# Optimization experiments

Hardware: AMD Instinct MI355X
Metric: run time of the kernel (lower is better)

The kernel has to match this reference:

```python
import jax, jax.numpy as jnp
import numpy as np

D_MODEL = 1024
D_FF = 4096
LN_EPS = 1e-5


def _layer_norm(x, gamma, beta):
    mu = jnp.mean(x, axis=-1, keepdims=True)
    var = jnp.mean(jnp.square(x - mu), axis=-1, keepdims=True)
    return (x - mu) * jax.lax.rsqrt(var + LN_EPS) * gamma + beta


def setup_inputs() -> dict:
    key = jax.random.key(0)
    ks = jax.random.split(key, 16)
    B, S, D, F = 2, 2048, D_MODEL, D_FF
    s_d = 1.0 / np.sqrt(D)
    s_f = 1.0 / np.sqrt(F)
    u = lambda k, shape, s: jax.random.uniform(k, shape, jnp.float32, -s, s)
    return {
        "x": jax.random.normal(ks[0], (B, S, D), jnp.float32),
        "wq": u(ks[1], (D, D), s_d), "bq": u(ks[2], (D,), s_d),
        "wk": u(ks[3], (D, D), s_d), "bk": u(ks[4], (D,), s_d),
        "wv": u(ks[5], (D, D), s_d), "bv": u(ks[6], (D,), s_d),
        "wo": u(ks[7], (D, D), s_d), "bo": u(ks[8], (D,), s_d),
        "w1": u(ks[9], (F, D), s_d), "b1": u(ks[10], (F,), s_d),
        "w2": u(ks[11], (D, F), s_f), "b2": u(ks[12], (D,), s_f),
        "g1": jnp.ones((D,), jnp.float32), "be1": jnp.zeros((D,), jnp.float32),
        "g2": jnp.ones((D,), jnp.float32), "be2": jnp.zeros((D,), jnp.float32),
        "num_heads": 16,
    }


def reference(x, wq, bq, wk, bk, wv, bv, wo, bo, w1, b1, w2, b2, g1, be1, g2, be2, num_heads):
    B, S, D = x.shape
    H = num_heads
    dk = D // H
    scale = 1.0 / np.sqrt(dk)

    # --- self-attention (pre-norm) ---
    h = _layer_norm(x, g1, be1)
    q = (h @ wq.T + bq).reshape(B, S, H, dk)
    k = (h @ wk.T + bk).reshape(B, S, H, dk)
    v = (h @ wv.T + bv).reshape(B, S, H, dk)
    scores = jnp.einsum("bqhd,bkhd->bhqk", q, k) * scale  # [B,H,S,S]
    attn = jax.nn.softmax(scores, axis=-1)
    ctx = jnp.einsum("bhqk,bkhd->bqhd", attn, v).reshape(B, S, D)
    x = x + ctx @ wo.T + bo

    # --- feed-forward (pre-norm, exact GELU as in torch default) ---
    h = _layer_norm(x, g2, be2)
    h = jax.nn.gelu(h @ w1.T + b1, approximate=False)
    x = x + h @ w2.T + b2
    return x
```

## Files before the change

### kernel.cpp

```cpp
#include <hip/hip_runtime.h>

typedef __attribute__((ext_vector_type(8))) __bf16 bf16x8;
typedef __attribute__((ext_vector_type(4))) __bf16 bf16x4;
typedef __attribute__((ext_vector_type(4))) float floatx4;
typedef void __attribute__((address_space(3))) lds_void_t;
typedef const void __attribute__((address_space(1))) gbl_void_t;

#define D_MODEL 1024
#define SEQ     2048
#define BATCH   2
#define NH      16
#define DK      64
#define DFF     4096
#define NTOK    (BATCH * SEQ)
#define QKVS    3072

#if __has_builtin(__builtin_amdgcn_exp2f)
#define EXP2(x) __builtin_amdgcn_exp2f(x)
#else
#define EXP2(x) exp2f(x)
#endif

__device__ __forceinline__ float gelu_exact(float x) {
    return 0.5f * x * (1.0f + erff(x * 0.70710678118654752f));
}

__global__ __launch_bounds__(256) void cast_f32_bf16(const float* __restrict__ src,
                                                     __bf16* __restrict__ dst, int n) {
    int i = (blockIdx.x * 256 + threadIdx.x) * 8;
    if (i >= n) return;
    floatx4 a = *(const floatx4*)(src + i);
    floatx4 b = *(const floatx4*)(src + i + 4);
    bf16x8 o;
    for (int j = 0; j < 4; ++j) { o[j] = (__bf16)a[j]; o[4 + j] = (__bf16)b[j]; }
    *(bf16x8*)(dst + i) = o;
}

__global__ __launch_bounds__(64) void ln_kernel(const float* __restrict__ x,
                                                const float* __restrict__ g,
                                                const float* __restrict__ b,
                                                __bf16* __restrict__ out) {
    int row = blockIdx.x, lane = threadIdx.x, base = lane * 16;
    const float* xr = x + (size_t)row * D_MODEL + base;
    float v[16];
    for (int j = 0; j < 4; ++j) {
        floatx4 a = *(const floatx4*)(xr + 4 * j);
        for (int i = 0; i < 4; ++i) v[4 * j + i] = a[i];
    }
    float s = 0.f, sq = 0.f;
    for (int i = 0; i < 16; ++i) { s += v[i]; sq += v[i] * v[i]; }
    for (int o = 1; o < 64; o <<= 1) { s += __shfl_xor(s, o); sq += __shfl_xor(sq, o); }
    float mu = s * (1.0f / D_MODEL);
    float var = sq * (1.0f / D_MODEL) - mu * mu;
    float rstd = rsqrtf(fmaxf(var, 0.f) + 1e-5f);

    const floatx4* gp = (const floatx4*)(g + base);
    const floatx4* bp = (const floatx4*)(b + base);
    bf16x8 o0, o1;
    for (int j = 0; j < 2; ++j) {
        floatx4 gv0 = gp[2 * j], gv1 = gp[2 * j + 1];
        floatx4 bv0 = bp[2 * j], bv1 = bp[2 * j + 1];
        for (int i = 0; i < 4; ++i) {
            float r0 = (v[8 * j + i] - mu) * rstd * gv0[i] + bv0[i];
            float r1 = (v[8 * j + 4 + i] - mu) * rstd * gv1[i] + bv1[i];
            if (j == 0) { o0[i] = (__bf16)r0; o0[4 + i] = (__bf16)r1; }
            else        { o1[i] = (__bf16)r0; o1[4 + i] = (__bf16)r1; }
        }
    }
    bf16x8* op = (bf16x8*)(out + (size_t)row * D_MODEL + base);
    op[0] = o0; op[1] = o1;
}

template <typename OutT, bool GELU, bool TRIBIAS, int KSPLIT>
__global__ __launch_bounds__(256) void gemm_bt(const __bf16* __restrict__ A,
                                               const __bf16* __restrict__ W,
                                               const float* __restrict__ bias0,
                                               const float* __restrict__ bias1,
                                               const float* __restrict__ bias2,
                                               const float* __restrict__ res,
                                               OutT* out, float* part1,
                                               int M, int N, int K) {
    __shared__ __bf16 As[2][128][32];
    __shared__ __bf16 Ws[2][128][32];

    int m0 = blockIdx.y * 128, n0 = blockIdx.x * 128;
    int t = threadIdx.x;
    int lane = t & 63, wave = t >> 6;
    int wm = (wave >> 1) * 64, wn = (wave & 1) * 64;
    int fr = lane & 15, quad = lane >> 4;
    int srow = t >> 2, scol = (t & 3) * 8;

    int Ks = K / KSPLIT;
    int kbeg = (KSPLIT > 1) ? blockIdx.z * Ks : 0;

    floatx4 acc[4][4] = {};

    const __bf16* Ab = A + (size_t)(m0 + srow) * K + kbeg + scol;
    const __bf16* Wb = W + (size_t)(n0 + srow) * K + kbeg + scol;

    auto stage = [&](int buf, int k0) {
        __builtin_amdgcn_global_load_lds((gbl_void_t*)(Ab + k0),
                                         (lds_void_t*)&As[buf][wave * 16][0], 16, 0, 0);
        __builtin_amdgcn_global_load_lds((gbl_void_t*)(Ab + (size_t)64 * K + k0),
                                         (lds_void_t*)&As[buf][64 + wave * 16][0], 16, 0, 0);
        __builtin_amdgcn_global_load_lds((gbl_void_t*)(Wb + k0),
                                         (lds_void_t*)&Ws[buf][wave * 16][0], 16, 0, 0);
        __builtin_amdgcn_global_load_lds((gbl_void_t*)(Wb + (size_t)64 * K + k0),
                                         (lds_void_t*)&Ws[buf][64 + wave * 16][0], 16, 0, 0);
    };

    stage(0, 0);
    int nsteps = Ks / 32;
    for (int s = 0; s < nsteps; ++s) {
        int cur = s & 1;
        __syncthreads();
        if (s + 1 < nsteps) stage(cur ^ 1, (s + 1) * 32);

        bf16x8 af[4], wf[4];
#pragma unroll
        for (int i = 0; i < 4; ++i) af[i] = *(const bf16x8*)&As[cur][wm + i * 16 + fr][quad * 8];
#pragma unroll
        for (int i = 0; i < 4; ++i) wf[i] = *(const bf16x8*)&Ws[cur][wn + i * 16 + fr][quad * 8];
#pragma unroll
        for (int mi = 0; mi < 4; ++mi)
#pragma unroll
            for (int ni = 0; ni < 4; ++ni)
                acc[mi][ni] = __builtin_amdgcn_mfma_f32_16x16x32_bf16(af[mi], wf[ni], acc[mi][ni], 0, 0, 0);
    }

    if (KSPLIT > 1) {
        float* pb = (blockIdx.z == 0) ? (float*)out : part1;
#pragma unroll
        for (int ni = 0; ni < 4; ++ni) {
            int col = n0 + wn + ni * 16 + fr;
#pragma unroll
            for (int mi = 0; mi < 4; ++mi)
#pragma unroll
                for (int r = 0; r < 4; ++r) {
                    int row = m0 + wm + mi * 16 + quad * 4 + r;
                    pb[(size_t)row * N + col] = acc[mi][ni][r];
                }
        }
    } else {
#pragma unroll
        for (int ni = 0; ni < 4; ++ni) {
            int col = n0 + wn + ni * 16 + fr;
            const float* bp = bias0;
            int bcol = col;
            if (TRIBIAS) { bp = col < 1024 ? bias0 : (col < 2048 ? bias1 : bias2); bcol = col & 1023; }
            float bv = bp[bcol];
#pragma unroll
            for (int mi = 0; mi < 4; ++mi) {
#pragma unroll
                for (int r = 0; r < 4; ++r) {
                    int row = m0 + wm + mi * 16 + quad * 4 + r;
                    float v = acc[mi][ni][r] + bv;
                    if (GELU) v = gelu_exact(v);
                    if (res) v += res[(size_t)row * N + col];
                    out[(size_t)row * N + col] = (OutT)v;
                }
            }
        }
    }
}

__global__ __launch_bounds__(256) void reduce_k2(const float* __restrict__ p0,
                                                 const float* p1,
                                                 const float* __restrict__ res,
                                                 const float* __restrict__ bias,
                                                 float* out) {
    int i = (blockIdx.x * 256 + threadIdx.x) * 4;
    floatx4 a = *(const floatx4*)(p0 + i);
    floatx4 b = *(const floatx4*)(p1 + i);
    floatx4 r = *(const floatx4*)(res + i);
    floatx4 bv = *(const floatx4*)(bias + (i & 1023));
    floatx4 o;
#pragma unroll
    for (int j = 0; j < 4; ++j) o[j] = a[j] + b[j] + r[j] + bv[j];
    *(floatx4*)(out + i) = o;
}

__global__ __launch_bounds__(256) void transpose_v(const __bf16* __restrict__ qkv,
                                                   __bf16* __restrict__ vt) {
    __shared__ __bf16 tile[64][72];
    int b = blockIdx.z, h = blockIdx.y, s0 = blockIdx.x * 64;
    int t = threadIdx.x;
    int dl = (t & 7) * 8, sl = t >> 3;
    for (int p = 0; p < 2; ++p) {
        int s = sl + p * 32;
        bf16x8 val = *(const bf16x8*)(qkv + (size_t)(b * SEQ + s0 + s) * QKVS + 2048 + h * DK + dl);
        *(bf16x8*)&tile[s][dl] = val;
    }
    __syncthreads();
    int sl2 = (t & 7) * 8, d = t >> 3;
    for (int p = 0; p < 2; ++p) {
        int dd = d + p * 32;
        bf16x8 val;
        for (int j = 0; j < 8; ++j) val[j] = tile[sl2 + j][dd];
        *(bf16x8*)(vt + ((size_t)(b * NH + h) * DK + dd) * SEQ + s0 + sl2) = val;
    }
}

__global__ __launch_bounds__(256, 2) void attn_kernel(const __bf16* __restrict__ qkv,
                                                      const __bf16* __restrict__ vt,
                                                      __bf16* __restrict__ ctx) {
    __shared__ __bf16 Klds[8192];
    __shared__ __bf16 Vlds[8192];
    __shared__ __bf16 Plds[4][16][136];
    int b = blockIdx.z, h = blockIdx.y;
    int wave = threadIdx.x >> 6, lane = threadIdx.x & 63;
    int q0 = blockIdx.x * 64 + wave * 16;
    int fr = lane & 15, quad = lane >> 4;
    const float sc2 = 0.18033688011112042f;

    const __bf16* qp = qkv + (size_t)(b * SEQ + q0 + fr) * QKVS + h * DK + quad * 8;
    bf16x8 qf0 = *(const bf16x8*)qp;
    bf16x8 qf1 = *(const bf16x8*)(qp + 32);

    const __bf16* kg = qkv + (size_t)b * SEQ * QKVS + 1024 + h * DK;
    const __bf16* vg = vt + (size_t)(b * NH + h) * DK * SEQ;

    floatx4 o[4] = {};
    float m_i = -1e30f, l_i = 0.f;

    auto stage_tile = [&](int k0) {
#pragma unroll
        for (int p = 0; p < 4; ++p) {
            int bid = wave * 4 + p;
            int f = bid >> 1, half = bid & 1;
            __builtin_amdgcn_global_load_lds(
                (gbl_void_t*)(kg + (size_t)(k0 + f * 16 + fr) * QKVS + quad * 8 + half * 32),
                (lds_void_t*)&Klds[bid * 512], 16, 0, 0);
            int c = bid >> 2, ti = bid & 3;
            __builtin_amdgcn_global_load_lds(
                (gbl_void_t*)(vg + (size_t)(ti * 16 + fr) * SEQ + k0 + c * 32 + quad * 8),
                (lds_void_t*)&Vlds[bid * 512], 16, 0, 0);
        }
    };

    stage_tile(0);
    __syncthreads();

    for (int k0 = 0; k0 < SEQ; k0 += 128) {
        const __bf16* Kb = Klds + lane * 8;
        const __bf16* Vb = Vlds + lane * 8;
        bf16x8 kA[8], kB[8];
#pragma unroll
        for (int f = 0; f < 8; ++f) {
            kA[f] = *(const bf16x8*)(Kb + (f * 2 + 0) * 512);
            kB[f] = *(const bf16x8*)(Kb + (f * 2 + 1) * 512);
        }
        bf16x8 vf[4][4];
#pragma unroll
        for (int c = 0; c < 4; ++c)
#pragma unroll
            for (int ti = 0; ti < 4; ++ti)
                vf[c][ti] = *(const bf16x8*)(Vb + (c * 4 + ti) * 512);
        __syncthreads();

        if (k0 + 128 < SEQ) stage_tile(k0 + 128);

        floatx4 s[8];
#pragma unroll
        for (int f = 0; f < 8; ++f) {
            floatx4 z = {0.f, 0.f, 0.f, 0.f};
            z = __builtin_amdgcn_mfma_f32_16x16x32_bf16(kA[f], qf0, z, 0, 0, 0);
            s[f] = __builtin_amdgcn_mfma_f32_16x16x32_bf16(kB[f], qf1, z, 0, 0, 0);
        }

        float fm[8];
#pragma unroll
        for (int f = 0; f < 8; ++f)
            fm[f] = fmaxf(fmaxf(s[f][0], s[f][1]), fmaxf(s[f][2], s[f][3]));
        float mx = fmaxf(fmaxf(fmaxf(fm[0], fm[1]), fmaxf(fm[2], fm[3])),
                         fmaxf(fmaxf(fm[4], fm[5]), fmaxf(fm[6], fm[7])));
        float mx2 = mx * sc2;
        mx2 = fmaxf(mx2, __shfl_xor(mx2, 16));
        mx2 = fmaxf(mx2, __shfl_xor(mx2, 32));
        float mn = fmaxf(m_i, mx2);
        float alpha = EXP2(m_i - mn);
        m_i = mn;
        float r0 = 0.f, r1 = 0.f, r2 = 0.f, r3 = 0.f;
#pragma unroll
        for (int f = 0; f < 8; ++f) {
            bf16x4 pk;
            float p0 = EXP2(fmaf(s[f][0], sc2, -mn));
            float p1 = EXP2(fmaf(s[f][1], sc2, -mn));
            float p2 = EXP2(fmaf(s[f][2], sc2, -mn));
            float p3 = EXP2(fmaf(s[f][3], sc2, -mn));
            r0 += p0; r1 += p1; r2 += p2; r3 += p3;
            pk[0] = (__bf16)p0; pk[1] = (__bf16)p1; pk[2] = (__bf16)p2; pk[3] = (__bf16)p3;
            *(bf16x4*)&Plds[wave][fr][f * 16 + quad * 4] = pk;
        }
        float rs = (r0 + r1) + (r2 + r3);
        rs += __shfl_xor(rs, 16);
        rs += __shfl_xor(rs, 32);
        l_i = l_i * alpha + rs;
        float aB[4];
#pragma unroll
        for (int r = 0; r < 4; ++r) aB[r] = __shfl(alpha, quad * 4 + r);
#pragma unroll
        for (int ti = 0; ti < 4; ++ti)
#pragma unroll
            for (int r = 0; r < 4; ++r) o[ti][r] *= aB[r];
        __threadfence_block();

        bf16x8 pa[4];
#pragma unroll
        for (int c = 0; c < 4; ++c)
            pa[c] = *(const bf16x8*)&Plds[wave][fr][c * 32 + quad * 8];
#pragma unroll
        for (int c = 0; c < 4; ++c)
#pragma unroll
            for (int ti = 0; ti < 4; ++ti)
                o[ti] = __builtin_amdgcn_mfma_f32_16x16x32_bf16(pa[c], vf[c][ti], o[ti], 0, 0, 0);
        __threadfence_block();

        __syncthreads();
    }
    float lB[4];
#pragma unroll
    for (int r = 0; r < 4; ++r) lB[r] = __shfl(l_i, quad * 4 + r);
#pragma unroll
    for (int ti = 0; ti < 4; ++ti)
#pragma unroll
        for (int r = 0; r < 4; ++r)
            ctx[(size_t)(b * SEQ + q0 + quad * 4 + r) * D_MODEL + h * DK + ti * 16 + fr] =
                (__bf16)(o[ti][r] / lB[r]);
}

extern "C" void kernel_launch(void* const* d_in, const int* in_sizes, int n_in,
                              void* d_out, int out_size, void* d_ws, size_t ws_size,
                              hipStream_t stream) {
    const float* x   = (const float*)d_in[0];
    const float* wq  = (const float*)d_in[1];
    const float* bq  = (const float*)d_in[2];
    const float* wk  = (const float*)d_in[3];
    const float* bk  = (const float*)d_in[4];
    const float* wv  = (const float*)d_in[5];
    const float* bv  = (const float*)d_in[6];
    const float* wo  = (const float*)d_in[7];
    const float* bo  = (const float*)d_in[8];
    const float* w1  = (const float*)d_in[9];
    const float* b1  = (const float*)d_in[10];
    const float* w2  = (const float*)d_in[11];
    const float* b2  = (const float*)d_in[12];
    const float* g1  = (const float*)d_in[13];
    const float* be1 = (const float*)d_in[14];
    const float* g2  = (const float*)d_in[15];
    const float* be2 = (const float*)d_in[16];
    float* out = (float*)d_out;

    char* ws = (char*)d_ws;
    const size_t MB = 1024 * 1024;
    __bf16* wqkvB = (__bf16*)(ws);
    __bf16* woB   = (__bf16*)(ws + 6 * MB);
    __bf16* w1B   = (__bf16*)(ws + 8 * MB);
    __bf16* w2B   = (__bf16*)(ws + 16 * MB);
    __bf16* h1    = (__bf16*)(ws + 24 * MB);
    float*  x1    = (float*)(ws + 24 * MB);
    __bf16* qkv   = (__bf16*)(ws + 40 * MB);
    __bf16* vt    = (__bf16*)(ws + 64 * MB);
    __bf16* ffh   = (__bf16*)(ws + 40 * MB);
    float*  pA0   = (float*)(ws + 40 * MB);
    float*  pA1   = (float*)(ws + 56 * MB);
    float*  pF0   = (float*)(ws);
    __bf16* ctx   = (__bf16*)d_out;
    __bf16* h2    = (__bf16*)d_out;

    const int NDD = D_MODEL * D_MODEL;
    const int NDF = D_MODEL * DFF;
    cast_f32_bf16<<<NDD / 2048, 256, 0, stream>>>(wq, wqkvB, NDD);
    cast_f32_bf16<<<NDD / 2048, 256, 0, stream>>>(wk, wqkvB + NDD, NDD);
    cast_f32_bf16<<<NDD / 2048, 256, 0, stream>>>(wv, wqkvB + 2 * NDD, NDD);
    cast_f32_bf16<<<NDD / 2048, 256, 0, stream>>>(wo, woB, NDD);
    cast_f32_bf16<<<NDF / 2048, 256, 0, stream>>>(w1, w1B, NDF);
    cast_f32_bf16<<<NDF / 2048, 256, 0, stream>>>(w2, w2B, NDF);

    dim3 gQKV(QKVS / 128, NTOK / 128);
    dim3 gDz(D_MODEL / 128, NTOK / 128, 2);
    dim3 gF(DFF / 128, NTOK / 128);
    dim3 gAttn(SEQ / 64, NH, BATCH);
    int gRed = NTOK * D_MODEL / (256 * 4);

    ln_kernel<<<NTOK, 64, 0, stream>>>(x, g1, be1, h1);
    gemm_bt<__bf16, false, true, 1><<<gQKV, 256, 0, stream>>>(h1, wqkvB, bq, bk, bv, nullptr, qkv, nullptr, NTOK, QKVS, D_MODEL);
    transpose_v<<<gAttn, 256, 0, stream>>>(qkv, vt);
    attn_kernel<<<gAttn, 256, 0, stream>>>(qkv, vt, ctx);
    gemm_bt<float, false, false, 2><<<gDz, 256, 0, stream>>>(ctx, woB, nullptr, nullptr, nullptr, nullptr, pA0, pA1, NTOK, D_MODEL, D_MODEL);
    reduce_k2<<<gRed, 256, 0, stream>>>(pA0, pA1, x, bo, x1);
    ln_kernel<<<NTOK, 64, 0, stream>>>(x1, g2, be2, h2);
    gemm_bt<__bf16, true, false, 1><<<gF, 256, 0, stream>>>(h2, w1B, b1, b1, b1, nullptr, ffh, nullptr, NTOK, DFF, D_MODEL);
    gemm_bt<float, false, false, 2><<<gDz, 256, 0, stream>>>(ffh, w2B, nullptr, nullptr, nullptr, nullptr, pF0, (float*)d_out, NTOK, D_MODEL, DFF);
    reduce_k2<<<gRed, 256, 0, stream>>>(pF0, (float*)d_out, x1, b2, out);
}
```

Measured before the change: 432.3 us.

## Process two 16-row query tiles per wave in attention to reuse K/V fragments

Each attention wave now handles 32 query rows as two 16-row subtiles instead of 16, so the block covers 128 queries and the grid halves. K and V fragments loaded from LDS per 128-key tile are reused across both subtiles, halving LDS and global K/V traffic per query. Part of the second subtile's QK MFMAs are placed before the barrier to overlap with the softmax. This raises register pressure (more accumulators and score arrays) and leaves fewer blocks (512) to fill the GPU.

```diff
diff --git a/kernel.cpp b/kernel.cpp
--- a/kernel.cpp
+++ b/kernel.cpp
@@ -206,22 +206,23 @@
                                                       __bf16* __restrict__ ctx) {
     __shared__ __bf16 Klds[8192];
     __shared__ __bf16 Vlds[8192];
-    __shared__ __bf16 Plds[4][16][136];
+    __shared__ __bf16 Plds[4][32][136];
     int b = blockIdx.z, h = blockIdx.y;
     int wave = threadIdx.x >> 6, lane = threadIdx.x & 63;
-    int q0 = blockIdx.x * 64 + wave * 16;
+    int q0 = blockIdx.x * 128 + wave * 32;
     int fr = lane & 15, quad = lane >> 4;
     const float sc2 = 0.18033688011112042f;
 
-    const __bf16* qp = qkv + (size_t)(b * SEQ + q0 + fr) * QKVS + h * DK + quad * 8;
-    bf16x8 qf0 = *(const bf16x8*)qp;
-    bf16x8 qf1 = *(const bf16x8*)(qp + 32);
+    const __bf16* qp0 = qkv + (size_t)(b * SEQ + q0 + fr) * QKVS + h * DK + quad * 8;
+    const __bf16* qp1 = qp0 + (size_t)16 * QKVS;
+    bf16x8 qA0 = *(const bf16x8*)qp0, qB0 = *(const bf16x8*)(qp0 + 32);
+    bf16x8 qA1 = *(const bf16x8*)qp1, qB1 = *(const bf16x8*)(qp1 + 32);
 
     const __bf16* kg = qkv + (size_t)b * SEQ * QKVS + 1024 + h * DK;
     const __bf16* vg = vt + (size_t)(b * NH + h) * DK * SEQ;
 
-    floatx4 o[4] = {};
-    float m_i = -1e30f, l_i = 0.f;
+    floatx4 o[8] = {};
+    float m0q = -1e30f, l0q = 0.f, m1q = -1e30f, l1q = 0.f;
 
     auto stage_tile = [&](int k0) {
 #pragma unroll
@@ -250,83 +251,141 @@
             kA[f] = *(const bf16x8*)(Kb + (f * 2 + 0) * 512);
             kB[f] = *(const bf16x8*)(Kb + (f * 2 + 1) * 512);
         }
+
+        floatx4 s[8];
+#pragma unroll
+        for (int f = 0; f < 8; ++f) {
+            floatx4 z = {0.f, 0.f, 0.f, 0.f};
+            z = __builtin_amdgcn_mfma_f32_16x16x32_bf16(kA[f], qA0, z, 0, 0, 0);
+            s[f] = __builtin_amdgcn_mfma_f32_16x16x32_bf16(kB[f], qB0, z, 0, 0, 0);
+        }
+        {
+            float fm[8];
+#pragma unroll
+            for (int f = 0; f < 8; ++f)
+                fm[f] = fmaxf(fmaxf(s[f][0], s[f][1]), fmaxf(s[f][2], s[f][3]));
+            float mx = fmaxf(fmaxf(fmaxf(fm[0], fm[1]), fmaxf(fm[2], fm[3])),
+                             fmaxf(fmaxf(fm[4], fm[5]), fmaxf(fm[6], fm[7])));
+            float mx2 = mx * sc2;
+            mx2 = fmaxf(mx2, __shfl_xor(mx2, 16));
+            mx2 = fmaxf(mx2, __shfl_xor(mx2, 32));
+            float mn = fmaxf(m0q, mx2);
+            float alpha = EXP2(m0q - mn);
+            m0q = mn;
+            float r0 = 0.f, r1 = 0.f, r2 = 0.f, r3 = 0.f;
+#pragma unroll
+            for (int f = 0; f < 8; ++f) {
+                bf16x4 pk;
+                float p0 = EXP2(fmaf(s[f][0], sc2, -mn));
+                float p1 = EXP2(fmaf(s[f][1], sc2, -mn));
+                float p2 = EXP2(fmaf(s[f][2], sc2, -mn));
+                float p3 = EXP2(fmaf(s[f][3], sc2, -mn));
+                r0 += p0; r1 += p1; r2 += p2; r3 += p3;
+                pk[0] = (__bf16)p0; pk[1] = (__bf16)p1; pk[2] = (__bf16)p2; pk[3] = (__bf16)p3;
+                *(bf16x4*)&Plds[wave][fr][f * 16 + quad * 4] = pk;
+            }
+            float rs = (r0 + r1) + (r2 + r3);
+            rs += __shfl_xor(rs, 16);
+            rs += __shfl_xor(rs, 32);
+            l0q = l0q * alpha + rs;
+            float aB[4];
+#pragma unroll
+            for (int r = 0; r < 4; ++r) aB[r] = __shfl(alpha, quad * 4 + r);
+#pragma unroll
+            for (int ti = 0; ti < 4; ++ti)
+#pragma unroll
+                for (int r = 0; r < 4; ++r) o[ti][r] *= aB[r];
+        }
+
+        floatx4 s1[8];
+#pragma unroll
+        for (int f = 0; f < 8; ++f) {
+            floatx4 z = {0.f, 0.f, 0.f, 0.f};
+            z = __builtin_amdgcn_mfma_f32_16x16x32_bf16(kA[f], qA1, z, 0, 0, 0);
+            s1[f] = __builtin_amdgcn_mfma_f32_16x16x32_bf16(kB[f], qB1, z, 0, 0, 0);
+        }
+
         bf16x8 vf[4][4];
 #pragma unroll
         for (int c = 0; c < 4; ++c)
 #pragma unroll
             for (int ti = 0; ti < 4; ++ti)
                 vf[c][ti] = *(const bf16x8*)(Vb + (c * 4 + ti) * 512);
+
         __syncthreads();
-
         if (k0 + 128 < SEQ) stage_tile(k0 + 128);
 
-        floatx4 s[8];
-#pragma unroll
-        for (int f = 0; f < 8; ++f) {
-            floatx4 z = {0.f, 0.f, 0.f, 0.f};
-            z = __builtin_amdgcn_mfma_f32_16x16x32_bf16(kA[f], qf0, z, 0, 0, 0);
-            s[f] = __builtin_amdgcn_mfma_f32_16x16x32_bf16(kB[f], qf1, z, 0, 0, 0);
-        }
-
-        float fm[8];
-#pragma unroll
-        for (int f = 0; f < 8; ++f)
-            fm[f] = fmaxf(fmaxf(s[f][0], s[f][1]), fmaxf(s[f][2], s[f][3]));
-        float mx = fmaxf(fmaxf(fmaxf(fm[0], fm[1]), fmaxf(fm[2], fm[3])),
-                         fmaxf(fmaxf(fm[4], fm[5]), fmaxf(fm[6], fm[7])));
-        float mx2 = mx * sc2;
-        mx2 = fmaxf(mx2, __shfl_xor(mx2, 16));
-        mx2 = fmaxf(mx2, __shfl_xor(mx2, 32));
-        float mn = fmaxf(m_i, mx2);
-        float alpha = EXP2(m_i - mn);
-        m_i = mn;
-        float r0 = 0.f, r1 = 0.f, r2 = 0.f, r3 = 0.f;
-#pragma unroll
-        for (int f = 0; f < 8; ++f) {
-            bf16x4 pk;
-            float p0 = EXP2(fmaf(s[f][0], sc2, -mn));
-            float p1 = EXP2(fmaf(s[f][1], sc2, -mn));
-            float p2 = EXP2(fmaf(s[f][2], sc2, -mn));
-            float p3 = EXP2(fmaf(s[f][3], sc2, -mn));
-            r0 += p0; r1 += p1; r2 += p2; r3 += p3;
-            pk[0] = (__bf16)p0; pk[1] = (__bf16)p1; pk[2] = (__bf16)p2; pk[3] = (__bf16)p3;
-            *(bf16x4*)&Plds[wave][fr][f * 16 + quad * 4] = pk;
-        }
-        float rs = (r0 + r1) + (r2 + r3);
-        rs += __shfl_xor(rs, 16);
-        rs += __shfl_xor(rs, 32);
-        l_i = l_i * alpha + rs;
-        float aB[4];
-#pragma unroll
-        for (int r = 0; r < 4; ++r) aB[r] = __shfl(alpha, quad * 4 + r);
-#pragma unroll
-        for (int ti = 0; ti < 4; ++ti)
-#pragma unroll
-            for (int r = 0; r < 4; ++r) o[ti][r] *= aB[r];
+        {
+            float fm[8];
+#pragma unroll
+            for (int f = 0; f < 8; ++f)
+                fm[f] = fmaxf(fmaxf(s1[f][0], s1[f][1]), fmaxf(s1[f][2], s1[f][3]));
+            float mx = fmaxf(fmaxf(fmaxf(fm[0], fm[1]), fmaxf(fm[2], fm[3])),
+                             fmaxf(fmaxf(fm[4], fm[5]), fmaxf(fm[6], fm[7])));
+            float mx2 = mx * sc2;
+            mx2 = fmaxf(mx2, __shfl_xor(mx2, 16));
+            mx2 = fmaxf(mx2, __shfl_xor(mx2, 32));
+            float mn = fmaxf(m1q, mx2);
+            float alpha = EXP2(m1q - mn);
+            m1q = mn;
+            float r0 = 0.f, r1 = 0.f, r2 = 0.f, r3 = 0.f;
+#pragma unroll
+            for (int f = 0; f < 8; ++f) {
+                bf16x4 pk;
+                float p0 = EXP2(fmaf(s1[f][0], sc2, -mn));
+                float p1 = EXP2(fmaf(s1[f][1], sc2, -mn));
+                float p2 = EXP2(fmaf(s1[f][2], sc2, -mn));
+                float p3 = EXP2(fmaf(s1[f][3], sc2, -mn));
+                r0 += p0; r1 += p1; r2 += p2; r3 += p3;
+                pk[0] = (__bf16)p0; pk[1] = (__bf16)p1; pk[2] = (__bf16)p2; pk[3] = (__bf16)p3;
+                *(bf16x4*)&Plds[wave][16 + fr][f * 16 + quad * 4] = pk;
+            }
+            float rs = (r0 + r1) + (r2 + r3);
+            rs += __shfl_xor(rs, 16);
+            rs += __shfl_xor(rs, 32);
+            l1q = l1q * alpha + rs;
+            float aB[4];
+#pragma unroll
+            for (int r = 0; r < 4; ++r) aB[r] = __shfl(alpha, quad * 4 + r);
+#pragma unroll
+            for (int ti = 0; ti < 4; ++ti)
+#pragma unroll
+                for (int r = 0; r < 4; ++r) o[4 + ti][r] *= aB[r];
+        }
         __threadfence_block();
 
-        bf16x8 pa[4];
+        bf16x8 pa0[4], pa1[4];
+#pragma unroll
+        for (int c = 0; c < 4; ++c) {
+            pa0[c] = *(const bf16x8*)&Plds[wave][fr][c * 32 + quad * 8];
+            pa1[c] = *(const bf16x8*)&Plds[wave][16 + fr][c * 32 + quad * 8];
+        }
 #pragma unroll
         for (int c = 0; c < 4; ++c)
-            pa[c] = *(const bf16x8*)&Plds[wave][fr][c * 32 + quad * 8];
-#pragma unroll
-        for (int c = 0; c < 4; ++c)
-#pragma unroll
-            for (int ti = 0; ti < 4; ++ti)
-                o[ti] = __builtin_amdgcn_mfma_f32_16x16x32_bf16(pa[c], vf[c][ti], o[ti], 0, 0, 0);
+#pragma unroll
+            for (int ti = 0; ti < 4; ++ti) {
+                o[ti]     = __builtin_amdgcn_mfma_f32_16x16x32_bf16(pa0[c], vf[c][ti], o[ti], 0, 0, 0);
+                o[4 + ti] = __builtin_amdgcn_mfma_f32_16x16x32_bf16(pa1[c], vf[c][ti], o[4 + ti], 0, 0, 0);
+            }
         __threadfence_block();
 
         __syncthreads();
     }
-    float lB[4];
-#pragma unroll
-    for (int r = 0; r < 4; ++r) lB[r] = __shfl(l_i, quad * 4 + r);
+    float lB0[4], lB1[4];
+#pragma unroll
+    for (int r = 0; r < 4; ++r) {
+        lB0[r] = __shfl(l0q, quad * 4 + r);
+        lB1[r] = __shfl(l1q, quad * 4 + r);
+    }
 #pragma unroll
     for (int ti = 0; ti < 4; ++ti)
 #pragma unroll
-        for (int r = 0; r < 4; ++r)
+        for (int r = 0; r < 4; ++r) {
             ctx[(size_t)(b * SEQ + q0 + quad * 4 + r) * D_MODEL + h * DK + ti * 16 + fr] =
-                (__bf16)(o[ti][r] / lB[r]);
+                (__bf16)(o[ti][r] / lB0[r]);
+            ctx[(size_t)(b * SEQ + q0 + 16 + quad * 4 + r) * D_MODEL + h * DK + ti * 16 + fr] =
+                (__bf16)(o[4 + ti][r] / lB1[r]);
+        }
 }
 
 extern "C" void kernel_launch(void* const* d_in, const int* in_sizes, int n_in,
@@ -380,12 +439,13 @@
     dim3 gQKV(QKVS / 128, NTOK / 128);
     dim3 gDz(D_MODEL / 128, NTOK / 128, 2);
     dim3 gF(DFF / 128, NTOK / 128);
-    dim3 gAttn(SEQ / 64, NH, BATCH);
+    dim3 gTr(SEQ / 64, NH, BATCH);
+    dim3 gAttn(SEQ / 128, NH, BATCH);
     int gRed = NTOK * D_MODEL / (256 * 4);
 
     ln_kernel<<<NTOK, 64, 0, stream>>>(x, g1, be1, h1);
     gemm_bt<__bf16, false, true, 1><<<gQKV, 256, 0, stream>>>(h1, wqkvB, bq, bk, bv, nullptr, qkv, nullptr, NTOK, QKVS, D_MODEL);
-    transpose_v<<<gAttn, 256, 0, stream>>>(qkv, vt);
+    transpose_v<<<gTr, 256, 0, stream>>>(qkv, vt);
     attn_kernel<<<gAttn, 256, 0, stream>>>(qkv, vt, ctx);
     gemm_bt<float, false, false, 2><<<gDz, 256, 0, stream>>>(ctx, woB, nullptr, nullptr, nullptr, nullptr, pA0, pA1, NTOK, D_MODEL, D_MODEL);
     reduce_k2<<<gRed, 256, 0, stream>>>(pA0, pA1, x, bo, x1);
```

Measured after the change: 417.7 us. -3.4%, faster.
